# Optimization experiments

Measured on AMD Instinct MI355X. Metric: run time of the kernel, lower is better.

The kernel has to match this reference:

```python
import jax, jax.numpy as jnp
from jax import lax
import numpy as np

N, C, H, W = 16, 128, 128, 128
CH = C // 4  # adapter contraction channels


def setup_inputs() -> dict:
    key = jax.random.key(0)
    ks = jax.random.split(key, 12)
    x = jax.random.normal(ks[0], (N, C, H, W), jnp.float32)
    # intensity in {1,2,3} as the torch module expects (intensity[i]-1 indexes adapters)
    intensity = jax.random.randint(ks[1], (N,), 1, 4)
    conv1_w = jax.random.normal(ks[2], (C, C, 3, 3), jnp.float32) * 0.02
    conv1_b = jnp.zeros((C,), jnp.float32)
    prelu1 = jnp.float32(0.25)  # nn.PReLU default single shared slope
    conv2_w = jax.random.normal(ks[3], (C, C, 3, 3), jnp.float32) * 0.02
    conv2_b = jnp.zeros((C,), jnp.float32)
    # 3 adapter experts, stacked on leading axis
    aW1 = jax.random.normal(ks[4], (3, CH, C), jnp.float32) * 0.05
    ab1 = jnp.zeros((3, CH), jnp.float32)
    aW2 = jax.random.normal(ks[5], (3, C, CH), jnp.float32) * 0.05
    ab2 = jnp.zeros((3, C), jnp.float32)
    prelu2 = jnp.float32(0.25)
    return dict(x=x, intensity=intensity, conv1_w=conv1_w, conv1_b=conv1_b,
                prelu1=prelu1, conv2_w=conv2_w, conv2_b=conv2_b,
                aW1=aW1, ab1=ab1, aW2=aW2, ab2=ab2, prelu2=prelu2)


def prelu(x, a):
    return jnp.where(x >= 0, x, a * x)


def conv3x3(x, w, b):
    y = lax.conv_general_dilated(x, w, window_strides=(1, 1),
                                 padding=((1, 1), (1, 1)),
                                 dimension_numbers=('NCHW', 'OIHW', 'NCHW'))
    return y + b[None, :, None, None]


def reference(x, intensity, conv1_w, conv1_b, prelu1, conv2_w, conv2_b,
              aW1, ab1, aW2, ab2, prelu2):
    h = prelu(conv3x3(x, conv1_w, conv1_b), prelu1)      # conv1 + PReLU
    h = conv3x3(h, conv2_w, conv2_b)                     # conv2, no activation
    x1 = jnp.mean(h, axis=(2, 3))                        # AdaptiveAvgPool2d(1)+Flatten -> [N,C]
    idx = intensity - 1                                  # expert id per sample
    W1, b1 = aW1[idx], ab1[idx]                          # gather per-sample expert weights
    W2, b2 = aW2[idx], ab2[idx]
    a = jax.nn.relu(jnp.einsum('nc,nhc->nh', x1, W1) + b1)
    g = jnp.einsum('nh,nch->nc', a, W2) + b2             # [N,C]
    out = h * jax.nn.sigmoid(g)[:, :, None, None] + x    # gated residual
    return prelu(out, prelu2)
```

## Files before the change

kernel.cpp:

```cpp
#include <hip/hip_runtime.h>
#include <hip/hip_bf16.h>
#include <math.h>

#define NN   16
#define C_   128
#define HH   128
#define WW   128
#define CHID 32
#define NTILES 64

typedef short bf16x8 __attribute__((ext_vector_type(8)));
typedef float f32x4  __attribute__((ext_vector_type(4)));

__device__ inline void glds16(const void* g, void* l) {
    __builtin_amdgcn_global_load_lds(
        (const __attribute__((address_space(1))) unsigned int*)g,
        (__attribute__((address_space(3))) unsigned int*)l, 16, 0, 0);
}

__device__ inline unsigned short f2bf(float f) {
    __hip_bfloat16 h = __float2bfloat16(f);
    return *reinterpret_cast<unsigned short*>(&h);
}

__global__ __launch_bounds__(64) void pack_w_k(
    const float* __restrict__ w1, const float* __restrict__ w2,
    unsigned short* __restrict__ wl)
{
    const int b = blockIdx.x;
    const int conv = b / 288, rem = b % 288;
    const int kk = rem / 32, ck = (rem % 32) / 8, cot = rem % 8;
    const int l = threadIdx.x;
    const int co  = cot * 16 + (l & 15);
    const int ci0 = ck * 32 + (l >> 4) * 8;
    const float* W = conv ? w2 : w1;
    union { unsigned short u[8]; uint4 v; } pk;
#pragma unroll
    for (int j = 0; j < 8; ++j)
        pk.u[j] = f2bf(W[(size_t)(co * C_ + ci0 + j) * 9 + kk]);
    unsigned short* dst = wl + (size_t)conv * 147456 +
        ((((size_t)kk * 4 + ck) * 8 + cot) * 64 + l) * 8;
    *reinterpret_cast<uint4*>(dst) = pk.v;
}

__global__ __launch_bounds__(256) void to_cnhwc_k(
    const float* __restrict__ x, unsigned short* __restrict__ xb)
{
    __shared__ unsigned short s_t[128][136];
    const int y = blockIdx.x, n = blockIdx.y, t = threadIdx.x;

#pragma unroll
    for (int p = 0; p < 16; ++p) {
        int fi = p * 256 + t;
        int ci = fi >> 5, x0 = (fi & 31) * 4;
        float4 v = *reinterpret_cast<const float4*>(
            x + (((size_t)(n * C_ + ci) * HH) + y) * WW + x0);
        s_t[x0 + 0][ci] = f2bf(v.x);
        s_t[x0 + 1][ci] = f2bf(v.y);
        s_t[x0 + 2][ci] = f2bf(v.z);
        s_t[x0 + 3][ci] = f2bf(v.w);
    }
    __syncthreads();
    unsigned short* dstbase = xb + ((size_t)(n * HH + y)) * 16384;
#pragma unroll
    for (int p = 0; p < 8; ++p) {
        int o = p * 256 + t;
        int ck = o >> 9, u = o & 511;
        int xc = u >> 2, ci0 = (u & 3) * 8;
        uint4 v = *reinterpret_cast<const uint4*>(&s_t[xc][ck * 32 + ci0]);
        *reinterpret_cast<uint4*>(dstbase + (size_t)ck * 4096 + xc * 32 + ci0) = v;
    }
}

template<int CONV>
__global__ __launch_bounds__(512) void conv_mfma_k(
    const unsigned short* __restrict__ inb,
    const unsigned short* __restrict__ wl,
    const float* __restrict__ bias,
    const float* __restrict__ prelu_a,
    unsigned short* __restrict__ outb,
    float* __restrict__ outf,
    float* __restrict__ partial)
{
    __shared__ unsigned short sB[4][132][32];
    __shared__ float s_part[8][64];

    const int tid = threadIdx.x;
    const int l = tid & 63, w = tid >> 6;
    const int wco = w >> 2, wy = (w >> 1) & 1, wxh = w & 1;
    const int lg = l >> 4, l15 = l & 15;
    const int yp = blockIdx.x, n = blockIdx.z;
    const int y0 = yp * 2;

    const f32x4 fz = {0.f, 0.f, 0.f, 0.f};
    f32x4 acc[4][4];
#pragma unroll
    for (int m = 0; m < 4; ++m)
#pragma unroll
        for (int nf = 0; nf < 4; ++nf) acc[m][nf] = fz;

    const bf16x8* wv = reinterpret_cast<const bf16x8*>(wl);
    char* sb0 = (char*)&sB[0][0][0];
    const uint4 z4 = {0u, 0u, 0u, 0u};

    for (int ck = 0; ck < 4; ++ck) {
        __syncthreads();
        {
            const int r = w >> 1, xh = w & 1;
            const int ygl = y0 - 1 + r;
            if (ygl < 0 || ygl >= HH) {
                int t2 = xh * 64 + l;
                for (int i = t2; i < 528; i += 128)
                    *reinterpret_cast<uint4*>(sb0 + r * 8448 + i * 16) = z4;
            } else {
                if (xh == 0 && l < 8) {
                    int col = (l < 4) ? 0 : 129, q = l & 3;
                    *reinterpret_cast<uint4*>(sb0 + r * 8448 + col * 64 + q * 16) = z4;
                }
                size_t rowbase = (((size_t)(n * HH + ygl)) * 4 + ck) * 8192;
#pragma unroll
                for (int i = 0; i < 4; ++i) {
                    const char* g = (const char*)inb + rowbase + xh * 4096 + i * 1024 + l * 16;
                    glds16(g, sb0 + r * 8448 + (1 + xh * 64 + i * 16) * 64);
                }
            }
        }
        __syncthreads();

        bf16x8 a_cur[4];
#pragma unroll
        for (int m = 0; m < 4; ++m)
            a_cur[m] = wv[(((size_t)0 * 4 + ck) * 8 + wco * 4 + m) * 64 + l];

#pragma unroll
        for (int kk = 0; kk < 9; ++kk) {
            const int ky = kk / 3, kx = kk % 3;
            bf16x8 a_nxt[4];
            if (kk < 8) {
#pragma unroll
                for (int m = 0; m < 4; ++m)
                    a_nxt[m] = wv[((((size_t)kk + 1) * 4 + ck) * 8 + wco * 4 + m) * 64 + l];
            }
            const int rrow = wy + ky;
            bf16x8 b[4];
#pragma unroll
            for (int nf = 0; nf < 4; ++nf) {
                int xi = wxh * 64 + nf * 16 + l15 + kx;
                b[nf] = *reinterpret_cast<const bf16x8*>(
                    sb0 + rrow * 8448 + xi * 64 + lg * 16);
            }
#pragma unroll
            for (int nf = 0; nf < 4; ++nf)
#pragma unroll
                for (int m = 0; m < 4; ++m)
                    acc[m][nf] = __builtin_amdgcn_mfma_f32_16x16x32_bf16(
                        a_cur[m], b[nf], acc[m][nf], 0, 0, 0);
            if (kk < 8) {
#pragma unroll
                for (int m = 0; m < 4; ++m) a_cur[m] = a_nxt[m];
            }
        }
    }

    const int ybase = y0 + wy;
    if (CONV == 1) {
        const float a1 = *prelu_a;
#pragma unroll
        for (int m = 0; m < 4; ++m) {
            const int co0 = wco * 64 + m * 16 + lg * 4;
            const int ck_out = wco * 2 + (m >> 1);
            const int cin = (m & 1) * 16 + lg * 4;
#pragma unroll
            for (int nf = 0; nf < 4; ++nf) {
                const int xc = wxh * 64 + nf * 16 + l15;
                union { unsigned short u[4]; uint2 v; } pk;
#pragma unroll
                for (int jj = 0; jj < 4; ++jj) {
                    float f = acc[m][nf][jj] + bias[co0 + jj];
                    f = (f >= 0.f) ? f : a1 * f;
                    pk.u[jj] = f2bf(f);
                }
                *reinterpret_cast<uint2*>(outb +
                    (((size_t)(n * HH + ybase)) * 4 + ck_out) * 4096 + xc * 32 + cin) = pk.v;
            }
        }
    } else {
        float ps[4][4];
#pragma unroll
        for (int m = 0; m < 4; ++m)
#pragma unroll
            for (int jj = 0; jj < 4; ++jj) ps[m][jj] = 0.f;
#pragma unroll
        for (int m = 0; m < 4; ++m) {
            const int co0 = wco * 64 + m * 16 + lg * 4;
#pragma unroll
            for (int nf = 0; nf < 4; ++nf) {
                const int xc = wxh * 64 + nf * 16 + l15;
#pragma unroll
                for (int jj = 0; jj < 4; ++jj) {
                    float f = acc[m][nf][jj] + bias[co0 + jj];
                    outf[(((size_t)(n * C_ + co0 + jj)) * HH + ybase) * WW + xc] = f;
                    ps[m][jj] += f;
                }
            }
        }
#pragma unroll
        for (int m = 0; m < 4; ++m)
#pragma unroll
            for (int jj = 0; jj < 4; ++jj) {
                float s = ps[m][jj];
                s += __shfl_xor(s, 1); s += __shfl_xor(s, 2);
                s += __shfl_xor(s, 4); s += __shfl_xor(s, 8);
                ps[m][jj] = s;
            }
        if (l15 == 0) {
#pragma unroll
            for (int m = 0; m < 4; ++m)
#pragma unroll
                for (int jj = 0; jj < 4; ++jj)
                    s_part[w][m * 16 + lg * 4 + jj] = ps[m][jj];
        }
        __syncthreads();
        if (tid < C_) {
            const int half = tid >> 6;
            float s = 0.f;
#pragma unroll
            for (int w2 = 0; w2 < 4; ++w2) s += s_part[half * 4 + w2][tid & 63];
            partial[((size_t)(n * C_ + tid)) * NTILES + yp] = s;
        }
    }
}

__global__ __launch_bounds__(C_) void adapter_k(
    const float* __restrict__ partial, const int* __restrict__ intensity,
    const float* __restrict__ aW1, const float* __restrict__ ab1,
    const float* __restrict__ aW2, const float* __restrict__ ab2,
    float* __restrict__ sig)
{
    __shared__ float sx[C_];
    __shared__ float sa[CHID];
    const int n = blockIdx.x, c = threadIdx.x;

    float s = 0.f;
    for (int t = 0; t < NTILES; ++t)
        s += partial[(size_t)(n * C_ + c) * NTILES + t];
    sx[c] = s * (1.f / (float)(HH * WW));
    __syncthreads();

    const int idx = intensity[n] - 1;
    if (c < CHID) {
        float a = ab1[idx * CHID + c];
        const float* wrow = aW1 + (size_t)(idx * CHID + c) * C_;
        for (int k = 0; k < C_; ++k) a = fmaf(wrow[k], sx[k], a);
        sa[c] = fmaxf(a, 0.f);
    }
    __syncthreads();

    float g = ab2[idx * C_ + c];
    const float* w2row = aW2 + (size_t)(idx * C_ + c) * CHID;
#pragma unroll
    for (int k = 0; k < CHID; ++k) g = fmaf(w2row[k], sa[k], g);
    sig[n * C_ + c] = 1.f / (1.f + expf(-g));
}

__global__ __launch_bounds__(256) void epilogue_k(
    const float* __restrict__ x, const float* __restrict__ sig,
    const float* __restrict__ prelu_a, float* __restrict__ out, int total4)
{
    const float a = *prelu_a;
    const int stride = gridDim.x * blockDim.x;
    for (int i = blockIdx.x * blockDim.x + threadIdx.x; i < total4; i += stride) {
        const int nc = (i * 4) >> 14;
        const float s = sig[nc];
        float4 h4 = ((const float4*)out)[i];
        float4 x4 = ((const float4*)x)[i];
        float4 v;
        v.x = h4.x * s + x4.x;  v.x = (v.x >= 0.f) ? v.x : a * v.x;
        v.y = h4.y * s + x4.y;  v.y = (v.y >= 0.f) ? v.y : a * v.y;
        v.z = h4.z * s + x4.z;  v.z = (v.z >= 0.f) ? v.z : a * v.z;
        v.w = h4.w * s + x4.w;  v.w = (v.w >= 0.f) ? v.w : a * v.w;
        ((float4*)out)[i] = v;
    }
}

extern "C" void kernel_launch(void* const* d_in, const int* in_sizes, int n_in,
                              void* d_out, int out_size, void* d_ws, size_t ws_size,
                              hipStream_t stream)
{
    const float* x         = (const float*)d_in[0];
    const int*   intensity = (const int*)  d_in[1];
    const float* w1        = (const float*)d_in[2];
    const float* b1        = (const float*)d_in[3];
    const float* p1        = (const float*)d_in[4];
    const float* w2        = (const float*)d_in[5];
    const float* b2        = (const float*)d_in[6];
    const float* aW1       = (const float*)d_in[7];
    const float* ab1       = (const float*)d_in[8];
    const float* aW2       = (const float*)d_in[9];
    const float* ab2       = (const float*)d_in[10];
    const float* p2        = (const float*)d_in[11];
    float* out = (float*)d_out;

    unsigned short* xb = (unsigned short*)d_out;

    unsigned short* h1b = (unsigned short*)d_ws;
    unsigned short* wl  = (unsigned short*)((char*)d_ws + (size_t)33554432 * 2);
    float* partial = (float*)((char*)wl + (size_t)294912 * 2);
    float* sig     = partial + (size_t)NN * C_ * NTILES;

    pack_w_k<<<dim3(576), dim3(64), 0, stream>>>(w1, w2, wl);
    to_cnhwc_k<<<dim3(HH, NN), dim3(256), 0, stream>>>(x, xb);

    conv_mfma_k<1><<<dim3(NTILES, 1, NN), dim3(512), 0, stream>>>(
        xb, wl, b1, p1, h1b, nullptr, nullptr);
    conv_mfma_k<2><<<dim3(NTILES, 1, NN), dim3(512), 0, stream>>>(
        h1b, wl + (size_t)147456, b2, nullptr, nullptr, out, partial);

    adapter_k<<<dim3(NN), dim3(C_), 0, stream>>>(
        partial, intensity, aW1, ab1, aW2, ab2, sig);

    const int total4 = NN * C_ * HH * WW / 4;
    epilogue_k<<<dim3(2048), dim3(256), 0, stream>>>(x, sig, p2, out, total4);
}
```

Before: 297.2 us.

## Swizzle LDS layouts to avoid bank conflicts and stage conv1 output via LDS

Applies XOR swizzles to the transpose kernel's shared tile and to the conv kernel's input row buffer, so that 16-byte LDS reads and writes spread across banks instead of colliding. The input swizzle is done by permuting global source addresses in global_load_lds, and the fragment reads apply the matching XOR. The conv1 epilogue now stages each output row through shared memory and writes 16-byte coalesced stores to the channel-blocked layout, replacing scattered 8-byte stores. This adds extra barriers and reuses the input buffer for the epilogue staging.

```diff
diff --git a/kernel.cpp b/kernel.cpp
--- a/kernel.cpp
+++ b/kernel.cpp
@@ -55,10 +55,11 @@
         int ci = fi >> 5, x0 = (fi & 31) * 4;
         float4 v = *reinterpret_cast<const float4*>(
             x + (((size_t)(n * C_ + ci) * HH) + y) * WW + x0);
-        s_t[x0 + 0][ci] = f2bf(v.x);
-        s_t[x0 + 1][ci] = f2bf(v.y);
-        s_t[x0 + 2][ci] = f2bf(v.z);
-        s_t[x0 + 3][ci] = f2bf(v.w);
+        const int slot = ((ci >> 3) ^ ((x0 >> 2) & 7)) * 8 + (ci & 7);
+        s_t[x0 + 0][slot] = f2bf(v.x);
+        s_t[x0 + 1][slot] = f2bf(v.y);
+        s_t[x0 + 2][slot] = f2bf(v.z);
+        s_t[x0 + 3][slot] = f2bf(v.w);
     }
     __syncthreads();
     unsigned short* dstbase = xb + ((size_t)(n * HH + y)) * 16384;
@@ -66,9 +67,11 @@
     for (int p = 0; p < 8; ++p) {
         int o = p * 256 + t;
         int ck = o >> 9, u = o & 511;
-        int xc = u >> 2, ci0 = (u & 3) * 8;
-        uint4 v = *reinterpret_cast<const uint4*>(&s_t[xc][ck * 32 + ci0]);
-        *reinterpret_cast<uint4*>(dstbase + (size_t)ck * 4096 + xc * 32 + ci0) = v;
+        int xc = u >> 2, q = u & 3;
+        int k = ck * 4 + q;
+        uint4 v = *reinterpret_cast<const uint4*>(
+            &s_t[xc][(k ^ ((xc >> 2) & 7)) * 8]);
+        *reinterpret_cast<uint4*>(dstbase + (size_t)ck * 4096 + xc * 32 + q * 8) = v;
     }
 }
 
@@ -82,7 +85,7 @@
     float* __restrict__ outf,
     float* __restrict__ partial)
 {
-    __shared__ unsigned short sB[4][132][32];
+    __shared__ char  smem[34816];
     __shared__ float s_part[8][64];
 
     const int tid = threadIdx.x;
@@ -100,7 +103,7 @@
         for (int nf = 0; nf < 4; ++nf) acc[m][nf] = fz;
 
     const bf16x8* wv = reinterpret_cast<const bf16x8*>(wl);
-    char* sb0 = (char*)&sB[0][0][0];
+    char* sb0 = smem;
     const uint4 z4 = {0u, 0u, 0u, 0u};
 
     for (int ck = 0; ck < 4; ++ck) {
@@ -120,7 +123,9 @@
                 size_t rowbase = (((size_t)(n * HH + ygl)) * 4 + ck) * 8192;
 #pragma unroll
                 for (int i = 0; i < 4; ++i) {
-                    const char* g = (const char*)inb + rowbase + xh * 4096 + i * 1024 + l * 16;
+                    const int p  = xh * 64 + i * 16 + (l >> 2);
+                    const int sd = (l & 3) ^ (((1 + p) >> 1) & 3);
+                    const char* g = (const char*)inb + rowbase + (size_t)p * 64 + sd * 16;
                     glds16(g, sb0 + r * 8448 + (1 + xh * 64 + i * 16) * 64);
                 }
             }
@@ -146,8 +151,9 @@
 #pragma unroll
             for (int nf = 0; nf < 4; ++nf) {
                 int xi = wxh * 64 + nf * 16 + l15 + kx;
+                int slot = lg ^ ((xi >> 1) & 3);
                 b[nf] = *reinterpret_cast<const bf16x8*>(
-                    sb0 + rrow * 8448 + xi * 64 + lg * 16);
+                    sb0 + rrow * 8448 + xi * 64 + slot * 16);
             }
 #pragma unroll
             for (int nf = 0; nf < 4; ++nf)
@@ -165,23 +171,37 @@
     const int ybase = y0 + wy;
     if (CONV == 1) {
         const float a1 = *prelu_a;
-#pragma unroll
-        for (int m = 0; m < 4; ++m) {
-            const int co0 = wco * 64 + m * 16 + lg * 4;
-            const int ck_out = wco * 2 + (m >> 1);
-            const int cin = (m & 1) * 16 + lg * 4;
-#pragma unroll
-            for (int nf = 0; nf < 4; ++nf) {
-                const int xc = wxh * 64 + nf * 16 + l15;
-                union { unsigned short u[4]; uint2 v; } pk;
-#pragma unroll
-                for (int jj = 0; jj < 4; ++jj) {
-                    float f = acc[m][nf][jj] + bias[co0 + jj];
-                    f = (f >= 0.f) ? f : a1 * f;
-                    pk.u[jj] = f2bf(f);
+        unsigned short (*s_rp)[136] = reinterpret_cast<unsigned short (*)[136]>(smem);
+        for (int r = 0; r < 2; ++r) {
+            __syncthreads();
+            if (wy == r) {
+#pragma unroll
+                for (int m = 0; m < 4; ++m) {
+                    const int co0 = wco * 64 + m * 16 + lg * 4;
+#pragma unroll
+                    for (int nf = 0; nf < 4; ++nf) {
+                        const int xc = wxh * 64 + nf * 16 + l15;
+                        union { unsigned short u[4]; uint2 v; } pk;
+#pragma unroll
+                        for (int jj = 0; jj < 4; ++jj) {
+                            float f = acc[m][nf][jj] + bias[co0 + jj];
+                            f = (f >= 0.f) ? f : a1 * f;
+                            pk.u[jj] = f2bf(f);
+                        }
+                        *reinterpret_cast<uint2*>(&s_rp[xc][co0]) = pk.v;
+                    }
                 }
-                *reinterpret_cast<uint2*>(outb +
-                    (((size_t)(n * HH + ybase)) * 4 + ck_out) * 4096 + xc * 32 + cin) = pk.v;
+            }
+            __syncthreads();
+            const int y = y0 + r;
+#pragma unroll
+            for (int p = 0; p < 4; ++p) {
+                int u = p * 512 + tid;
+                int xc = u >> 4, k = u & 15;
+                uint4 v = *reinterpret_cast<const uint4*>(&s_rp[xc][k * 8]);
+                *reinterpret_cast<uint4*>(outb +
+                    (((size_t)(n * HH + y)) * 4 + (k >> 2)) * 4096 +
+                    xc * 32 + (k & 3) * 8) = v;
             }
         }
     } else {
```

After: 275.3 us. -7.4%, faster.
